# Performance work log

Hardware: AMD Instinct MI355X
Metric: run time of the kernel (lower is better)

## Reference

```python
import jax, jax.numpy as jnp
import numpy as np

N, B, T, D = 4, 4, 512, 512
H, DK, DV = 8, 64, 64
LN_EPS = 1e-5


def setup_inputs() -> dict:
    key = jax.random.key(0)
    ks = jax.random.split(key, 5)
    s = 1.0 / np.sqrt(D)
    return {
        "x": jax.random.normal(ks[0], (N, B, T, D), jnp.float32),
        "Wq": jax.random.normal(ks[1], (D, H * DK), jnp.float32) * s,
        "bq": jnp.zeros((H * DK,), jnp.float32),
        "Wk": jax.random.normal(ks[2], (D, H * DK), jnp.float32) * s,
        "bk": jnp.zeros((H * DK,), jnp.float32),
        "Wv": jax.random.normal(ks[3], (D, H * DV), jnp.float32) * s,
        "bv": jnp.zeros((H * DV,), jnp.float32),
        "Wo": jax.random.normal(ks[4], (H * DV, D), jnp.float32) * (1.0 / np.sqrt(H * DV)),
        "bo": jnp.zeros((D,), jnp.float32),
        "gamma": jnp.ones((D,), jnp.float32),
        "beta": jnp.zeros((D,), jnp.float32),
    }


def reference(x, Wq, bq, Wk, bk, Wv, bv, Wo, bo, gamma, beta):
    # x: [N, B, T, D] -- N variables, each [B, T, D]
    n = x.shape[0]
    # Project once per variable (the torch code redundantly recomputes K/V per query var).
    q = (x @ Wq + bq).reshape(n, B, T, H, DK).transpose(0, 1, 3, 2, 4)  # [N,B,H,T,DK]
    k = (x @ Wk + bk).reshape(n, B, T, H, DK).transpose(0, 1, 3, 2, 4)  # [N,B,H,T,DK]
    v = (x @ Wv + bv).reshape(n, B, T, H, DV).transpose(0, 1, 3, 2, 4)  # [N,B,H,T,DV]
    # All-pairs attention: softmax over keys of EACH key-variable separately.
    scores = jnp.einsum('qbhtk,cbhsk->qcbhts', q, k) / np.sqrt(DK)  # [Nq,Nc,B,H,T,T]
    attn = jax.nn.softmax(scores, axis=-1)
    ctx = jnp.einsum('qcbhts,cbhsv->qcbhtv', attn, v)  # [Nq,Nc,B,H,T,DV]
    ctx = ctx.transpose(0, 1, 2, 4, 3, 5).reshape(n, n, B, T, H * DV)
    out = ctx @ Wo + bo                     # per-pair output projection
    out = out.sum(axis=1) / n               # average over key variables -> [N,B,T,D]
    res = x + out
    mu = res.mean(axis=-1, keepdims=True)
    var = res.var(axis=-1, keepdims=True)
    y = (res - mu) / jnp.sqrt(var + LN_EPS) * gamma + beta
    return y
```

## Files before the change

### kernel.cpp

```cpp
#include <hip/hip_runtime.h>


typedef __bf16 bf16x8 __attribute__((ext_vector_type(8)));
typedef __bf16 bf16x4 __attribute__((ext_vector_type(4)));
typedef short shortx4 __attribute__((ext_vector_type(4)));
typedef float floatx4 __attribute__((ext_vector_type(4)));
typedef float floatx16 __attribute__((ext_vector_type(16)));
typedef unsigned short ushortx8 __attribute__((ext_vector_type(8)));

static __device__ __forceinline__ unsigned short f2bf(float f) {
  union { __bf16 h; unsigned short u; } c; c.h = (__bf16)f; return c.u;
}
static __device__ __forceinline__ float bf2f(unsigned short u) {
  union { unsigned u32; float f; } c; c.u32 = ((unsigned)u) << 16; return c.f;
}

#define QSCALE 0.18033688011112042f
#define SHIFT2 (-17.312340489609306f)

__global__ __launch_bounds__(256) void prep(
    const float* __restrict__ Wq, const float* __restrict__ Wk,
    const float* __restrict__ Wv, const float* __restrict__ Wo,
    const float* __restrict__ x,
    unsigned short* __restrict__ wqkvT, unsigned short* __restrict__ woT,
    unsigned short* __restrict__ x_bf)
{
  const int bid = blockIdx.x;
  const int tid = threadIdx.x;
  if (bid < 256) {
    __shared__ unsigned short lds[64][65];
    const int z = bid >> 6, rest = bid & 63;
    const int k0 = (rest >> 3) * 64, n0 = (rest & 7) * 64;
    const float* W; unsigned short* T;
    if (z == 0)      { W = Wq; T = wqkvT; }
    else if (z == 1) { W = Wk; T = wqkvT + 262144; }
    else if (z == 2) { W = Wv; T = wqkvT + 524288; }
    else             { W = Wo; T = woT; }
    const int xx = tid & 63, yy = tid >> 6;
#pragma unroll
    for (int i = 0; i < 16; ++i) {
      const int row = yy * 16 + i;
      lds[row][xx] = f2bf(W[(size_t)(k0 + row) * 512 + n0 + xx]);
    }
    __syncthreads();
#pragma unroll
    for (int i = 0; i < 16; ++i) {
      const int nr = yy * 16 + i;
      T[(size_t)(n0 + nr) * 512 + k0 + xx] = lds[xx][nr];
    }
  } else {
    const int i = (bid - 256) * 256 + tid;
    const float4 a = ((const float4*)x)[i * 2];
    const float4 b = ((const float4*)x)[i * 2 + 1];
    ushortx8 o;
    o[0] = f2bf(a.x); o[1] = f2bf(a.y); o[2] = f2bf(a.z); o[3] = f2bf(a.w);
    o[4] = f2bf(b.x); o[5] = f2bf(b.y); o[6] = f2bf(b.z); o[7] = f2bf(b.w);
    *(ushortx8*)(x_bf + (size_t)i * 8) = o;
  }
}

__global__ __launch_bounds__(256) void gemm_qkv(
    const unsigned short* __restrict__ Xb,
    const unsigned short* __restrict__ BT,
    const float* __restrict__ bq, const float* __restrict__ bk,
    const float* __restrict__ bv,
    unsigned short* __restrict__ Qo, unsigned short* __restrict__ Ko,
    unsigned short* __restrict__ Vo)
{
  __shared__ __align__(16) unsigned short sbuf[18432];
  auto lA = (unsigned short (*)[72])sbuf;
  auto lB = (unsigned short (*)[72])(sbuf + 9216);
  const int tid  = threadIdx.x;
  const int wv   = tid >> 6, lane = tid & 63;
  const int quad = lane >> 4, l16 = lane & 15;
  const int wm = wv >> 1, wn = wv & 1;
  const int m0  = blockIdx.x * 128;
  const int n0g = blockIdx.y * 128;
  const int sel = n0g >> 9;
  const float* bias = (sel == 0) ? bq : (sel == 1) ? bk : bv;
  const float scale = (sel == 0) ? QSCALE : 1.0f;
  unsigned short* outp = (sel == 0) ? Qo : (sel == 1) ? Ko : Vo;

  floatx4 acc[4][4] = {};
  const int srow = tid >> 1, sc0 = (tid & 1) * 32;

  for (int kc = 0; kc < 512; kc += 64) {
    __syncthreads();
    const unsigned short* as = Xb + (size_t)(m0 + srow) * 512 + kc + sc0;
    const unsigned short* bs = BT + (size_t)(n0g + srow) * 512 + kc + sc0;
#pragma unroll
    for (int j = 0; j < 4; ++j) {
      *(bf16x8*)&lA[srow][sc0 + j * 8] = *(const bf16x8*)(as + j * 8);
      *(bf16x8*)&lB[srow][sc0 + j * 8] = *(const bf16x8*)(bs + j * 8);
    }
    __syncthreads();
    bf16x8 af[4][2];
#pragma unroll
    for (int ti = 0; ti < 4; ++ti) {
      af[ti][0] = *(const bf16x8*)&lA[wm * 64 + ti * 16 + l16][quad * 8];
      af[ti][1] = *(const bf16x8*)&lA[wm * 64 + ti * 16 + l16][32 + quad * 8];
    }
#pragma unroll
    for (int ni = 0; ni < 4; ++ni) {
      bf16x8 b0 = *(const bf16x8*)&lB[wn * 64 + ni * 16 + l16][quad * 8];
      bf16x8 b1 = *(const bf16x8*)&lB[wn * 64 + ni * 16 + l16][32 + quad * 8];
#pragma unroll
      for (int ti = 0; ti < 4; ++ti) {
        acc[ti][ni] = __builtin_amdgcn_mfma_f32_16x16x32_bf16(af[ti][0], b0, acc[ti][ni], 0, 0, 0);
        acc[ti][ni] = __builtin_amdgcn_mfma_f32_16x16x32_bf16(af[ti][1], b1, acc[ti][ni], 0, 0, 0);
      }
    }
  }

  if (sel != 2) {
#pragma unroll
    for (int ni = 0; ni < 4; ++ni) {
      const int n = (n0g & 511) + wn * 64 + ni * 16 + l16;
      const float bvv = bias[n];
      const int hh = n >> 6, dk = n & 63;
#pragma unroll
      for (int ti = 0; ti < 4; ++ti) {
        const int mb = m0 + wm * 64 + ti * 16 + quad * 4;
#pragma unroll
        for (int r = 0; r < 4; ++r) {
          const int m = mb + r;
          const int nb = m >> 9, t = m & 511;
          outp[((size_t)(nb * 8 + hh) * 512 + t) * 64 + dk] =
              f2bf((acc[ti][ni][r] + bvv) * scale);
        }
      }
    }
  } else {
    __syncthreads();
    auto tb = (unsigned short (*)[136])sbuf;
#pragma unroll
    for (int ni = 0; ni < 4; ++ni) {
      const int n = (n0g & 511) + wn * 64 + ni * 16 + l16;
      const float bvv = bias[n];
      const int drow = wn * 64 + ni * 16 + l16;
#pragma unroll
      for (int ti = 0; ti < 4; ++ti) {
        const int tcol = wm * 64 + ti * 16 + quad * 4;
        shortx4 pk;
        pk[0] = (short)f2bf(acc[ti][ni][0] + bvv);
        pk[1] = (short)f2bf(acc[ti][ni][1] + bvv);
        pk[2] = (short)f2bf(acc[ti][ni][2] + bvv);
        pk[3] = (short)f2bf(acc[ti][ni][3] + bvv);
        *(shortx4*)&tb[drow][tcol] = pk;
      }
    }
    __syncthreads();
    const int drow = tid >> 1, th = tid & 1;
    const int n = (n0g & 511) + drow;
    const int hh = n >> 6, dk = n & 63;
    const int nb = m0 >> 9, tbase = (m0 & 511) + th * 64;
    unsigned short* gdst = outp + ((size_t)(nb * 8 + hh) * 64 + dk) * 512 + tbase;
#pragma unroll
    for (int j = 0; j < 8; ++j)
      *(ushortx8*)(gdst + j * 8) = *(const ushortx8*)&tb[drow][th * 64 + j * 8];
  }
}

__global__ __launch_bounds__(256) void gemm_out(
    const unsigned short* __restrict__ C0, const unsigned short* __restrict__ C1,
    const unsigned short* __restrict__ BT, unsigned short* __restrict__ Cout)
{
  __shared__ __align__(16) unsigned short lA[128][72];
  __shared__ __align__(16) unsigned short lB[128][72];
  const int tid  = threadIdx.x;
  const int wv   = tid >> 6, lane = tid & 63;
  const int quad = lane >> 4, l16 = lane & 15;
  const int wm = wv >> 1, wn = wv & 1;
  const int m0 = blockIdx.x * 128, n0 = blockIdx.y * 128;

  floatx4 acc[4][4] = {};
  const int srow = tid >> 1, sc0 = (tid & 1) * 32;

  for (int kc = 0; kc < 512; kc += 64) {
    __syncthreads();
    const size_t aoff = (size_t)(m0 + srow) * 512 + kc + sc0;
    const unsigned short* bs = BT + (size_t)(n0 + srow) * 512 + kc + sc0;
#pragma unroll
    for (int j = 0; j < 4; ++j) {
      ushortx8 a0 = *(const ushortx8*)(C0 + aoff + j * 8);
      ushortx8 a1 = *(const ushortx8*)(C1 + aoff + j * 8);
      ushortx8 o;
#pragma unroll
      for (int e = 0; e < 8; ++e) o[e] = f2bf(bf2f(a0[e]) + bf2f(a1[e]));
      *(ushortx8*)&lA[srow][sc0 + j * 8] = o;
      *(bf16x8*)&lB[srow][sc0 + j * 8] = *(const bf16x8*)(bs + j * 8);
    }
    __syncthreads();
    bf16x8 af[4][2];
#pragma unroll
    for (int ti = 0; ti < 4; ++ti) {
      af[ti][0] = *(const bf16x8*)&lA[wm * 64 + ti * 16 + l16][quad * 8];
      af[ti][1] = *(const bf16x8*)&lA[wm * 64 + ti * 16 + l16][32 + quad * 8];
    }
#pragma unroll
    for (int ni = 0; ni < 4; ++ni) {
      bf16x8 b0 = *(const bf16x8*)&lB[wn * 64 + ni * 16 + l16][quad * 8];
      bf16x8 b1 = *(const bf16x8*)&lB[wn * 64 + ni * 16 + l16][32 + quad * 8];
#pragma unroll
      for (int ti = 0; ti < 4; ++ti) {
        acc[ti][ni] = __builtin_amdgcn_mfma_f32_16x16x32_bf16(af[ti][0], b0, acc[ti][ni], 0, 0, 0);
        acc[ti][ni] = __builtin_amdgcn_mfma_f32_16x16x32_bf16(af[ti][1], b1, acc[ti][ni], 0, 0, 0);
      }
    }
  }

#pragma unroll
  for (int ni = 0; ni < 4; ++ni) {
    const int n = n0 + wn * 64 + ni * 16 + l16;
#pragma unroll
    for (int ti = 0; ti < 4; ++ti) {
      const int mb = m0 + wm * 64 + ti * 16 + quad * 4;
#pragma unroll
      for (int r = 0; r < 4; ++r)
        Cout[(size_t)(mb + r) * 512 + n] = f2bf(acc[ti][ni][r]);
    }
  }
}

__global__ __launch_bounds__(256) void flash_kernel(
    const unsigned short* __restrict__ Q,
    const unsigned short* __restrict__ K,
    const unsigned short* __restrict__ VT,
    unsigned short* __restrict__ CTX2)
{
  __shared__ __align__(16) unsigned short lK[2][64][72];
  __shared__ __align__(16) unsigned short lV[2][64][68];
  const int tid  = threadIdx.x;
  const int wv   = tid >> 6, lane = tid & 63;
  const int l32  = lane & 31, u = lane >> 5;

  const int lin  = blockIdx.x;
  const int xcd  = lin & 7, slot = lin >> 3;
  const int tile = slot & 3;
  const int nbh  = xcd * 16 + ((slot >> 2) & 15);
  const int cg   = slot >> 6;
  const int t0   = tile * 128;
  const int h = nbh & 7, nb = nbh >> 3, b = nb & 3;

  const unsigned short* qbase = Q + ((size_t)nbh * 512 + (t0 + wv * 32 + l32)) * 64;
  bf16x8 qf[4];
#pragma unroll
  for (int c16 = 0; c16 < 4; ++c16)
    qf[c16] = *(const bf16x8*)(qbase + c16 * 16 + u * 8);

  const int srow = tid >> 2, sc0 = (tid & 3) * 16;
  const unsigned short *kptr, *vptr;
  auto setptr = [&](int it) {
    const int c = cg * 2 + (it >> 3), s0 = (it & 7) * 64;
    const size_t kvbh = (size_t)((c * 4 + b) * 8 + h);
    kptr = K  + kvbh * (512 * 64) + (size_t)(s0 + srow) * 64 + sc0;
    vptr = VT + kvbh * (64 * 512) + (size_t)srow * 512 + s0 + sc0;
  };
  bf16x8 rk0, rk1, rv0, rv1;
  auto loadregs = [&]() {
    rk0 = *(const bf16x8*)kptr; rk1 = *(const bf16x8*)(kptr + 8);
    rv0 = *(const bf16x8*)vptr; rv1 = *(const bf16x8*)(vptr + 8);
  };
  auto writebuf = [&](int p) {
    *(bf16x8*)&lK[p][srow][sc0]     = rk0;
    *(bf16x8*)&lK[p][srow][sc0 + 8] = rk1;
    union { bf16x8 v8; bf16x4 v4[2]; } c0, c1;
    c0.v8 = rv0; c1.v8 = rv1;
    *(bf16x4*)&lV[p][srow][sc0]      = c0.v4[0];
    *(bf16x4*)&lV[p][srow][sc0 + 4]  = c0.v4[1];
    *(bf16x4*)&lV[p][srow][sc0 + 8]  = c1.v4[0];
    *(bf16x4*)&lV[p][srow][sc0 + 12] = c1.v4[1];
  };

  setptr(0); loadregs();
  writebuf(0);
  setptr(1); loadregs();
  __syncthreads();

  floatx16 ofin0 = {}, ofin1 = {};
  floatx16 oc0, oc1;
  float lacc;

  for (int it = 0; it < 16; ++it) {
    const int cur = it & 1;
    const int st = it & 7;
    if (st == 0) { oc0 = floatx16{}; oc1 = floatx16{}; lacc = 0.f; }

    if (it < 15) writebuf(cur ^ 1);
    if (it < 14) { setptr(it + 2); loadregs(); }

    floatx16 sacc0, sacc1;
#pragma unroll
    for (int r = 0; r < 16; ++r) { sacc0[r] = SHIFT2; sacc1[r] = SHIFT2; }
#pragma unroll
    for (int c16 = 0; c16 < 4; ++c16) {
      bf16x8 ak0 = *(const bf16x8*)&lK[cur][l32][c16 * 16 + u * 8];
      bf16x8 ak1 = *(const bf16x8*)&lK[cur][32 + l32][c16 * 16 + u * 8];
      sacc0 = __builtin_amdgcn_mfma_f32_32x32x16_bf16(ak0, qf[c16], sacc0, 0, 0, 0);
      sacc1 = __builtin_amdgcn_mfma_f32_32x32x16_bf16(ak1, qf[c16], sacc1, 0, 0, 0);
    }

#pragma unroll
    for (int sb = 0; sb < 2; ++sb) {
      const floatx16& sa = sb ? sacc1 : sacc0;
#pragma unroll
      for (int c8 = 0; c8 < 4; ++c8) {
        float e0 = __builtin_amdgcn_exp2f(sa[4 * c8 + 0]);
        float e1 = __builtin_amdgcn_exp2f(sa[4 * c8 + 1]);
        float e2 = __builtin_amdgcn_exp2f(sa[4 * c8 + 2]);
        float e3 = __builtin_amdgcn_exp2f(sa[4 * c8 + 3]);
        lacc += (e0 + e1) + (e2 + e3);
        shortx4 pf;
        pf[0] = (short)f2bf(e0); pf[1] = (short)f2bf(e1);
        pf[2] = (short)f2bf(e2); pf[3] = (short)f2bf(e3);
        const int sloc = sb * 32 + c8 * 8 + u * 4;
        shortx4 vf0 = *(const shortx4*)&lV[cur][l32][sloc];
        shortx4 vf1 = *(const shortx4*)&lV[cur][32 + l32][sloc];
        oc0 = __builtin_amdgcn_mfma_f32_32x32x8bf16_1k(pf, vf0, oc0, 0, 0, 0);
        oc1 = __builtin_amdgcn_mfma_f32_32x32x8bf16_1k(pf, vf1, oc1, 0, 0, 0);
      }
    }

    if (st == 7) {
      float s = lacc;
      s += __shfl_xor(s, 32);
      const float inv = 1.0f / s;
#pragma unroll
      for (int r = 0; r < 16; ++r) {
        const int trow = (r & 3) + 8 * (r >> 2) + 4 * u;
        const float invr = __shfl(inv, trow);
        ofin0[r] += oc0[r] * invr;
        ofin1[r] += oc1[r] * invr;
      }
    }
    __syncthreads();
  }

  unsigned short* outp = CTX2 + (size_t)cg * (8192 * 512);
  const int mbase = nb * 512 + t0 + wv * 32;
#pragma unroll
  for (int r = 0; r < 16; ++r) {
    const int trow = (r & 3) + 8 * (r >> 2) + 4 * u;
    const size_t rowoff = (size_t)(mbase + trow) * 512 + h * 64;
    outp[rowoff + l32]      = f2bf(ofin0[r]);
    outp[rowoff + 32 + l32] = f2bf(ofin1[r]);
  }
}

__global__ __launch_bounds__(256) void ln_kernel(
    const float* __restrict__ x, const unsigned short* __restrict__ tmpb,
    const float* __restrict__ bo, const float* __restrict__ gamma,
    const float* __restrict__ beta, float* __restrict__ out)
{
  const int wv   = threadIdx.x >> 6, lane = threadIdx.x & 63;
  const int row  = blockIdx.x * 4 + wv;
  const int col  = lane * 8;
  const size_t base = (size_t)row * 512 + col;
  const float4 x0 = *(const float4*)(x + base);
  const float4 x1 = *(const float4*)(x + base + 4);
  const ushortx8 t8 = *(const ushortx8*)(tmpb + base);
  const float4 b0 = *(const float4*)(bo + col);
  const float4 b1 = *(const float4*)(bo + col + 4);
  float r[8];
  r[0] = x0.x + 0.25f * bf2f(t8[0]) + b0.x;  r[1] = x0.y + 0.25f * bf2f(t8[1]) + b0.y;
  r[2] = x0.z + 0.25f * bf2f(t8[2]) + b0.z;  r[3] = x0.w + 0.25f * bf2f(t8[3]) + b0.w;
  r[4] = x1.x + 0.25f * bf2f(t8[4]) + b1.x;  r[5] = x1.y + 0.25f * bf2f(t8[5]) + b1.y;
  r[6] = x1.z + 0.25f * bf2f(t8[6]) + b1.z;  r[7] = x1.w + 0.25f * bf2f(t8[7]) + b1.w;
  float s = 0.f, sq = 0.f;
#pragma unroll
  for (int j = 0; j < 8; ++j) { s += r[j]; sq += r[j] * r[j]; }
#pragma unroll
  for (int off = 1; off < 64; off <<= 1) {
    s  += __shfl_xor(s, off);
    sq += __shfl_xor(sq, off);
  }
  const float mu  = s * (1.0f / 512.0f);
  const float var = sq * (1.0f / 512.0f) - mu * mu;
  const float inv = rsqrtf(var + 1e-5f);
  const float4 g0 = *(const float4*)(gamma + col);
  const float4 g1 = *(const float4*)(gamma + col + 4);
  const float4 be0 = *(const float4*)(beta + col);
  const float4 be1 = *(const float4*)(beta + col + 4);
  float4 o0, o1;
  o0.x = (r[0] - mu) * inv * g0.x + be0.x;  o0.y = (r[1] - mu) * inv * g0.y + be0.y;
  o0.z = (r[2] - mu) * inv * g0.z + be0.z;  o0.w = (r[3] - mu) * inv * g0.w + be0.w;
  o1.x = (r[4] - mu) * inv * g1.x + be1.x;  o1.y = (r[5] - mu) * inv * g1.y + be1.y;
  o1.z = (r[6] - mu) * inv * g1.z + be1.z;  o1.w = (r[7] - mu) * inv * g1.w + be1.w;
  *(float4*)(out + base)     = o0;
  *(float4*)(out + base + 4) = o1;
}

extern "C" void kernel_launch(void* const* d_in, const int* in_sizes, int n_in,
                              void* d_out, int out_size, void* d_ws, size_t ws_size,
                              hipStream_t stream) {
  const float* x     = (const float*)d_in[0];
  const float* Wq    = (const float*)d_in[1];
  const float* bq    = (const float*)d_in[2];
  const float* Wk    = (const float*)d_in[3];
  const float* bk    = (const float*)d_in[4];
  const float* Wv    = (const float*)d_in[5];
  const float* bv    = (const float*)d_in[6];
  const float* Wo    = (const float*)d_in[7];
  const float* bo    = (const float*)d_in[8];
  const float* gamma = (const float*)d_in[9];
  const float* beta  = (const float*)d_in[10];
  float* out = (float*)d_out;

  char* w = (char*)d_ws;
  unsigned short* q_bf  = (unsigned short*)(w);
  unsigned short* k_bf  = (unsigned short*)(w + (size_t)8  * 1024 * 1024);
  unsigned short* vt_bf = (unsigned short*)(w + (size_t)16 * 1024 * 1024);
  unsigned short* x_bf  = (unsigned short*)(w + (size_t)24 * 1024 * 1024);
  unsigned short* ctx2  = (unsigned short*)(w + (size_t)24 * 1024 * 1024);
  unsigned short* wqkvT = (unsigned short*)(w + (size_t)40 * 1024 * 1024);
  unsigned short* woT   = wqkvT + 786432;
  unsigned short* tmpb  = (unsigned short*)(w);

  prep<<<2304, 256, 0, stream>>>(Wq, Wk, Wv, Wo, x, wqkvT, woT, x_bf);
  gemm_qkv<<<dim3(64, 12), 256, 0, stream>>>(x_bf, wqkvT, bq, bk, bv,
                                             q_bf, k_bf, vt_bf);
  flash_kernel<<<1024, 256, 0, stream>>>(q_bf, k_bf, vt_bf, ctx2);
  gemm_out<<<dim3(64, 4), 256, 0, stream>>>(ctx2, ctx2 + (size_t)8192 * 512,
                                            woT, tmpb);
  ln_kernel<<<2048, 256, 0, stream>>>(x, tmpb, bo, gamma, beta, out);
}
```

Measured before the change: 196.8 us.

## Use direct global-to-LDS loads in GEMMs and wider MFMA for PV

```diff
diff --git a/kernel.cpp b/kernel.cpp
--- a/kernel.cpp
+++ b/kernel.cpp
@@ -4,6 +4,7 @@
 typedef __bf16 bf16x8 __attribute__((ext_vector_type(8)));
 typedef __bf16 bf16x4 __attribute__((ext_vector_type(4)));
 typedef short shortx4 __attribute__((ext_vector_type(4)));
+typedef short shortx8 __attribute__((ext_vector_type(8)));
 typedef float floatx4 __attribute__((ext_vector_type(4)));
 typedef float floatx16 __attribute__((ext_vector_type(16)));
 typedef unsigned short ushortx8 __attribute__((ext_vector_type(8)));
@@ -14,6 +15,10 @@
 static __device__ __forceinline__ float bf2f(unsigned short u) {
   union { unsigned u32; float f; } c; c.u32 = ((unsigned)u) << 16; return c.f;
 }
+
+#define GLOAD16(gp, lp) __builtin_amdgcn_global_load_lds( \
+    (const __attribute__((address_space(1))) void*)(gp),  \
+    (__attribute__((address_space(3))) void*)(lp), 16, 0, 0)
 
 #define QSCALE 0.18033688011112042f
 #define SHIFT2 (-17.312340489609306f)
@@ -67,9 +72,9 @@
     unsigned short* __restrict__ Qo, unsigned short* __restrict__ Ko,
     unsigned short* __restrict__ Vo)
 {
-  __shared__ __align__(16) unsigned short sbuf[18432];
-  auto lA = (unsigned short (*)[72])sbuf;
-  auto lB = (unsigned short (*)[72])(sbuf + 9216);
+  __shared__ __align__(16) unsigned short sbuf[17408];
+  unsigned short* sA = sbuf;
+  unsigned short* sB = sbuf + 8192;
   const int tid  = threadIdx.x;
   const int wv   = tid >> 6, lane = tid & 63;
   const int quad = lane >> 4, l16 = lane & 15;
@@ -82,28 +87,28 @@
   unsigned short* outp = (sel == 0) ? Qo : (sel == 1) ? Ko : Vo;
 
   floatx4 acc[4][4] = {};
-  const int srow = tid >> 1, sc0 = (tid & 1) * 32;
 
   for (int kc = 0; kc < 512; kc += 64) {
     __syncthreads();
-    const unsigned short* as = Xb + (size_t)(m0 + srow) * 512 + kc + sc0;
-    const unsigned short* bs = BT + (size_t)(n0g + srow) * 512 + kc + sc0;
-#pragma unroll
-    for (int j = 0; j < 4; ++j) {
-      *(bf16x8*)&lA[srow][sc0 + j * 8] = *(const bf16x8*)(as + j * 8);
-      *(bf16x8*)&lB[srow][sc0 + j * 8] = *(const bf16x8*)(bs + j * 8);
+#pragma unroll
+    for (int i = 0; i < 4; ++i) {
+      const int ib  = (wv * 4 + i) * 512;
+      const int o   = ib + lane * 8;
+      const int row = o >> 6, col = o & 63;
+      GLOAD16(Xb + (size_t)(m0  + row) * 512 + kc + col, sA + ib);
+      GLOAD16(BT + (size_t)(n0g + row) * 512 + kc + col, sB + ib);
     }
     __syncthreads();
     bf16x8 af[4][2];
 #pragma unroll
     for (int ti = 0; ti < 4; ++ti) {
-      af[ti][0] = *(const bf16x8*)&lA[wm * 64 + ti * 16 + l16][quad * 8];
-      af[ti][1] = *(const bf16x8*)&lA[wm * 64 + ti * 16 + l16][32 + quad * 8];
+      af[ti][0] = *(const bf16x8*)&sA[(wm * 64 + ti * 16 + l16) * 64 + quad * 8];
+      af[ti][1] = *(const bf16x8*)&sA[(wm * 64 + ti * 16 + l16) * 64 + 32 + quad * 8];
     }
 #pragma unroll
     for (int ni = 0; ni < 4; ++ni) {
-      bf16x8 b0 = *(const bf16x8*)&lB[wn * 64 + ni * 16 + l16][quad * 8];
-      bf16x8 b1 = *(const bf16x8*)&lB[wn * 64 + ni * 16 + l16][32 + quad * 8];
+      bf16x8 b0 = *(const bf16x8*)&sB[(wn * 64 + ni * 16 + l16) * 64 + quad * 8];
+      bf16x8 b1 = *(const bf16x8*)&sB[(wn * 64 + ni * 16 + l16) * 64 + 32 + quad * 8];
 #pragma unroll
       for (int ti = 0; ti < 4; ++ti) {
         acc[ti][ni] = __builtin_amdgcn_mfma_f32_16x16x32_bf16(af[ti][0], b0, acc[ti][ni], 0, 0, 0);
@@ -166,7 +171,7 @@
     const unsigned short* __restrict__ BT, unsigned short* __restrict__ Cout)
 {
   __shared__ __align__(16) unsigned short lA[128][72];
-  __shared__ __align__(16) unsigned short lB[128][72];
+  __shared__ __align__(16) unsigned short sB[8192];
   const int tid  = threadIdx.x;
   const int wv   = tid >> 6, lane = tid & 63;
   const int quad = lane >> 4, l16 = lane & 15;
@@ -178,17 +183,22 @@
 
   for (int kc = 0; kc < 512; kc += 64) {
     __syncthreads();
+#pragma unroll
+    for (int i = 0; i < 4; ++i) {
+      const int ib  = (wv * 4 + i) * 512;
+      const int o   = ib + lane * 8;
+      const int row = o >> 6, col = o & 63;
+      GLOAD16(BT + (size_t)(n0 + row) * 512 + kc + col, sB + ib);
+    }
     const size_t aoff = (size_t)(m0 + srow) * 512 + kc + sc0;
-    const unsigned short* bs = BT + (size_t)(n0 + srow) * 512 + kc + sc0;
 #pragma unroll
     for (int j = 0; j < 4; ++j) {
       ushortx8 a0 = *(const ushortx8*)(C0 + aoff + j * 8);
       ushortx8 a1 = *(const ushortx8*)(C1 + aoff + j * 8);
-      ushortx8 o;
-#pragma unroll
-      for (int e = 0; e < 8; ++e) o[e] = f2bf(bf2f(a0[e]) + bf2f(a1[e]));
-      *(ushortx8*)&lA[srow][sc0 + j * 8] = o;
-      *(bf16x8*)&lB[srow][sc0 + j * 8] = *(const bf16x8*)(bs + j * 8);
+      ushortx8 o8;
+#pragma unroll
+      for (int e = 0; e < 8; ++e) o8[e] = f2bf(bf2f(a0[e]) + bf2f(a1[e]));
+      *(ushortx8*)&lA[srow][sc0 + j * 8] = o8;
     }
     __syncthreads();
     bf16x8 af[4][2];
@@ -199,8 +209,8 @@
     }
 #pragma unroll
     for (int ni = 0; ni < 4; ++ni) {
-      bf16x8 b0 = *(const bf16x8*)&lB[wn * 64 + ni * 16 + l16][quad * 8];
-      bf16x8 b1 = *(const bf16x8*)&lB[wn * 64 + ni * 16 + l16][32 + quad * 8];
+      bf16x8 b0 = *(const bf16x8*)&sB[(wn * 64 + ni * 16 + l16) * 64 + quad * 8];
+      bf16x8 b1 = *(const bf16x8*)&sB[(wn * 64 + ni * 16 + l16) * 64 + 32 + quad * 8];
 #pragma unroll
       for (int ti = 0; ti < 4; ++ti) {
         acc[ti][ni] = __builtin_amdgcn_mfma_f32_16x16x32_bf16(af[ti][0], b0, acc[ti][ni], 0, 0, 0);
@@ -304,20 +314,22 @@
     for (int sb = 0; sb < 2; ++sb) {
       const floatx16& sa = sb ? sacc1 : sacc0;
 #pragma unroll
-      for (int c8 = 0; c8 < 4; ++c8) {
-        float e0 = __builtin_amdgcn_exp2f(sa[4 * c8 + 0]);
-        float e1 = __builtin_amdgcn_exp2f(sa[4 * c8 + 1]);
-        float e2 = __builtin_amdgcn_exp2f(sa[4 * c8 + 2]);
-        float e3 = __builtin_amdgcn_exp2f(sa[4 * c8 + 3]);
-        lacc += (e0 + e1) + (e2 + e3);
-        shortx4 pf;
-        pf[0] = (short)f2bf(e0); pf[1] = (short)f2bf(e1);
-        pf[2] = (short)f2bf(e2); pf[3] = (short)f2bf(e3);
-        const int sloc = sb * 32 + c8 * 8 + u * 4;
-        shortx4 vf0 = *(const shortx4*)&lV[cur][l32][sloc];
-        shortx4 vf1 = *(const shortx4*)&lV[cur][32 + l32][sloc];
-        oc0 = __builtin_amdgcn_mfma_f32_32x32x8bf16_1k(pf, vf0, oc0, 0, 0, 0);
-        oc1 = __builtin_amdgcn_mfma_f32_32x32x8bf16_1k(pf, vf1, oc1, 0, 0, 0);
+      for (int g = 0; g < 2; ++g) {
+        float e[8];
+#pragma unroll
+        for (int j = 0; j < 8; ++j) e[j] = __builtin_amdgcn_exp2f(sa[8 * g + j]);
+        lacc += ((e[0] + e[1]) + (e[2] + e[3])) + ((e[4] + e[5]) + (e[6] + e[7]));
+        union { shortx8 s8; bf16x8 b8; } pf;
+#pragma unroll
+        for (int j = 0; j < 8; ++j) pf.s8[j] = (short)f2bf(e[j]);
+        const int slA = sb * 32 + g * 16 + u * 4;
+        union { shortx4 s4[2]; bf16x8 b8; } va, vb;
+        va.s4[0] = *(const shortx4*)&lV[cur][l32][slA];
+        va.s4[1] = *(const shortx4*)&lV[cur][l32][slA + 8];
+        vb.s4[0] = *(const shortx4*)&lV[cur][32 + l32][slA];
+        vb.s4[1] = *(const shortx4*)&lV[cur][32 + l32][slA + 8];
+        oc0 = __builtin_amdgcn_mfma_f32_32x32x16_bf16(pf.b8, va.b8, oc0, 0, 0, 0);
+        oc1 = __builtin_amdgcn_mfma_f32_32x32x16_bf16(pf.b8, vb.b8, oc1, 0, 0, 0);
       }
     }
 
```

Measured after the change: 194.0 us. No clear change (-1.4%).

## Use 32x32x16 MFMA for PV, packed bf16 convert, and setprio

Applied to the files above, without the earlier changes.

```diff
diff --git a/kernel.cpp b/kernel.cpp
--- a/kernel.cpp
+++ b/kernel.cpp
@@ -4,15 +4,23 @@
 typedef __bf16 bf16x8 __attribute__((ext_vector_type(8)));
 typedef __bf16 bf16x4 __attribute__((ext_vector_type(4)));
 typedef short shortx4 __attribute__((ext_vector_type(4)));
+typedef short shortx8 __attribute__((ext_vector_type(8)));
+typedef float floatx2 __attribute__((ext_vector_type(2)));
 typedef float floatx4 __attribute__((ext_vector_type(4)));
 typedef float floatx16 __attribute__((ext_vector_type(16)));
 typedef unsigned short ushortx8 __attribute__((ext_vector_type(8)));
+typedef unsigned int uintx4 __attribute__((ext_vector_type(4)));
 
 static __device__ __forceinline__ unsigned short f2bf(float f) {
   union { __bf16 h; unsigned short u; } c; c.h = (__bf16)f; return c.u;
 }
 static __device__ __forceinline__ float bf2f(unsigned short u) {
   union { unsigned u32; float f; } c; c.u32 = ((unsigned)u) << 16; return c.f;
+}
+static __device__ __forceinline__ unsigned cvtpk(float a, float b) {
+  unsigned r;
+  asm("v_cvt_pk_bf16_f32 %0, %1, %2" : "=v"(r) : "v"(a), "v"(b));
+  return r;
 }
 
 #define QSCALE 0.18033688011112042f
@@ -277,23 +285,32 @@
   setptr(1); loadregs();
   __syncthreads();
 
+  floatx16 shiftC;
+#pragma unroll
+  for (int r = 0; r < 16; ++r) shiftC[r] = SHIFT2;
+
   floatx16 ofin0 = {}, ofin1 = {};
   floatx16 oc0, oc1;
-  float lacc;
+  floatx2 lac2;
 
   for (int it = 0; it < 16; ++it) {
     const int cur = it & 1;
     const int st = it & 7;
-    if (st == 0) { oc0 = floatx16{}; oc1 = floatx16{}; lacc = 0.f; }
+    if (st == 0) { oc0 = floatx16{}; oc1 = floatx16{}; lac2 = floatx2{}; }
 
     if (it < 15) writebuf(cur ^ 1);
     if (it < 14) { setptr(it + 2); loadregs(); }
 
+    __builtin_amdgcn_s_setprio(1);
     floatx16 sacc0, sacc1;
-#pragma unroll
-    for (int r = 0; r < 16; ++r) { sacc0[r] = SHIFT2; sacc1[r] = SHIFT2; }
-#pragma unroll
-    for (int c16 = 0; c16 < 4; ++c16) {
+    {
+      bf16x8 ak0 = *(const bf16x8*)&lK[cur][l32][u * 8];
+      bf16x8 ak1 = *(const bf16x8*)&lK[cur][32 + l32][u * 8];
+      sacc0 = __builtin_amdgcn_mfma_f32_32x32x16_bf16(ak0, qf[0], shiftC, 0, 0, 0);
+      sacc1 = __builtin_amdgcn_mfma_f32_32x32x16_bf16(ak1, qf[0], shiftC, 0, 0, 0);
+    }
+#pragma unroll
+    for (int c16 = 1; c16 < 4; ++c16) {
       bf16x8 ak0 = *(const bf16x8*)&lK[cur][l32][c16 * 16 + u * 8];
       bf16x8 ak1 = *(const bf16x8*)&lK[cur][32 + l32][c16 * 16 + u * 8];
       sacc0 = __builtin_amdgcn_mfma_f32_32x32x16_bf16(ak0, qf[c16], sacc0, 0, 0, 0);
@@ -304,25 +321,32 @@
     for (int sb = 0; sb < 2; ++sb) {
       const floatx16& sa = sb ? sacc1 : sacc0;
 #pragma unroll
-      for (int c8 = 0; c8 < 4; ++c8) {
-        float e0 = __builtin_amdgcn_exp2f(sa[4 * c8 + 0]);
-        float e1 = __builtin_amdgcn_exp2f(sa[4 * c8 + 1]);
-        float e2 = __builtin_amdgcn_exp2f(sa[4 * c8 + 2]);
-        float e3 = __builtin_amdgcn_exp2f(sa[4 * c8 + 3]);
-        lacc += (e0 + e1) + (e2 + e3);
-        shortx4 pf;
-        pf[0] = (short)f2bf(e0); pf[1] = (short)f2bf(e1);
-        pf[2] = (short)f2bf(e2); pf[3] = (short)f2bf(e3);
-        const int sloc = sb * 32 + c8 * 8 + u * 4;
-        shortx4 vf0 = *(const shortx4*)&lV[cur][l32][sloc];
-        shortx4 vf1 = *(const shortx4*)&lV[cur][32 + l32][sloc];
-        oc0 = __builtin_amdgcn_mfma_f32_32x32x8bf16_1k(pf, vf0, oc0, 0, 0, 0);
-        oc1 = __builtin_amdgcn_mfma_f32_32x32x8bf16_1k(pf, vf1, oc1, 0, 0, 0);
-      }
-    }
+      for (int g = 0; g < 2; ++g) {
+        float e[8];
+#pragma unroll
+        for (int j = 0; j < 8; ++j) e[j] = __builtin_amdgcn_exp2f(sa[8 * g + j]);
+        floatx2 s01 = floatx2{e[0], e[1]} + floatx2{e[2], e[3]};
+        floatx2 s23 = floatx2{e[4], e[5]} + floatx2{e[6], e[7]};
+        lac2 += s01 + s23;
+        union { unsigned u32[4]; bf16x8 b8; } pf;
+        pf.u32[0] = cvtpk(e[0], e[1]);
+        pf.u32[1] = cvtpk(e[2], e[3]);
+        pf.u32[2] = cvtpk(e[4], e[5]);
+        pf.u32[3] = cvtpk(e[6], e[7]);
+        const int slA = sb * 32 + g * 16 + u * 4;
+        union { shortx4 s4[2]; bf16x8 b8; } va, vb;
+        va.s4[0] = *(const shortx4*)&lV[cur][l32][slA];
+        va.s4[1] = *(const shortx4*)&lV[cur][l32][slA + 8];
+        vb.s4[0] = *(const shortx4*)&lV[cur][32 + l32][slA];
+        vb.s4[1] = *(const shortx4*)&lV[cur][32 + l32][slA + 8];
+        oc0 = __builtin_amdgcn_mfma_f32_32x32x16_bf16(pf.b8, va.b8, oc0, 0, 0, 0);
+        oc1 = __builtin_amdgcn_mfma_f32_32x32x16_bf16(pf.b8, vb.b8, oc1, 0, 0, 0);
+      }
+    }
+    __builtin_amdgcn_s_setprio(0);
 
     if (st == 7) {
-      float s = lacc;
+      float s = lac2[0] + lac2[1];
       s += __shfl_xor(s, 32);
       const float inv = 1.0f / s;
 #pragma unroll
```

Result: faster. 189.6 us (-3.7%).
